# Kernel tuning notes

Measured on AMD Instinct MI355X. Metric: run time of the kernel, lower is better.

Reference implementation:

```python
import jax, jax.numpy as jnp
import numpy as np


def _spectral_norm(W, u):
    # W: [out, in] (1x1 conv weight flattened), u: [out]
    # one power-iteration step (torch does this under no_grad), then
    # sigma = u' @ W @ v with gradient flowing through W only.
    v = W.T @ u
    v = v / jnp.linalg.norm(v)
    u2 = W @ v
    u2 = u2 / jnp.linalg.norm(u2)
    v = jax.lax.stop_gradient(v)
    u2 = jax.lax.stop_gradient(u2)
    sigma = u2 @ (W @ v)
    return W / sigma


def setup_inputs() -> dict:
    key = jax.random.key(0)
    ks = jax.random.split(key, 8)
    B, C, H, W = 32, 512, 32, 32
    Cq = C // 8  # 64
    x = jax.random.normal(ks[0], (B, C, H, W), dtype=jnp.float32)
    s = 1.0 / np.sqrt(C)
    return {
        "x": x,
        "Wq": jax.random.normal(ks[1], (Cq, C), dtype=jnp.float32) * s,
        "bq": jnp.zeros((Cq,), dtype=jnp.float32),
        "uq": jax.random.normal(ks[2], (Cq,), dtype=jnp.float32),
        "Wk": jax.random.normal(ks[3], (Cq, C), dtype=jnp.float32) * s,
        "bk": jnp.zeros((Cq,), dtype=jnp.float32),
        "uk": jax.random.normal(ks[4], (Cq,), dtype=jnp.float32),
        "Wv": jax.random.normal(ks[5], (C, C), dtype=jnp.float32) * s,
        "bv": jnp.zeros((C,), dtype=jnp.float32),
        "uv": jax.random.normal(ks[6], (C,), dtype=jnp.float32),
        "gamma": jnp.float32(0.5),
    }


def reference(x, Wq, bq, uq, Wk, bk, uk, Wv, bv, uv, gamma):
    B, C, H, W = x.shape
    N = H * W
    f = x.reshape(B, C, N)                                   # [B,C,N]
    # 1x1 conv == channel matmul with spectral-normalized weights
    q = jnp.einsum('oc,bcn->bno', _spectral_norm(Wq, uq), f) + bq          # [B,N,Cq]
    k = jnp.einsum('oc,bcn->bon', _spectral_norm(Wk, uk), f) + bk[:, None]  # [B,Cq,N]
    v = jnp.einsum('oc,bcn->bon', _spectral_norm(Wv, uv), f) + bv[:, None]  # [B,C,N]
    qk = jnp.einsum('bno,bom->bnm', q, k)                    # [B,N,N], no 1/sqrt(d)
    attn = jax.nn.softmax(qk, axis=1)                        # softmax over QUERY axis (dim 1)
    o = jnp.einsum('bcn,bnm->bcm', v, attn).reshape(B, C, H, W)
    return gamma * o + x
```

## Files before the change

### kernel.cpp

```cpp
#include <hip/hip_runtime.h>
#include <hip/hip_bf16.h>

typedef __hip_bfloat16 bf16;
typedef __bf16 bf16x8 __attribute__((ext_vector_type(8)));
typedef float  f32x4  __attribute__((ext_vector_type(4)));
typedef unsigned short u16x8 __attribute__((ext_vector_type(8)));

#define C_IN  512
#define N_SP  1024
#define BATCH 32

__device__ __forceinline__ float ldmix(const void* p, size_t i, int f32) {
    return f32 ? ((const float*)p)[i] : __bfloat162float(((const bf16*)p)[i]);
}
__device__ __forceinline__ void stmix(void* p, size_t i, float v, int f32) {
    if (f32) ((float*)p)[i] = v;
    else     ((bf16*)p)[i] = __float2bfloat16(v);
}
__device__ __forceinline__ unsigned short bfbits(float f) {
    bf16 t = __float2bfloat16(f);
    return *reinterpret_cast<unsigned short*>(&t);
}
__device__ __forceinline__ float bf2f(unsigned short h) {
    union { unsigned u; float f; } c; c.u = ((unsigned)h) << 16; return c.f;
}
__device__ __forceinline__ void ldvec8(const void* W, size_t base, int f32, float v[8]) {
    if (f32) {
        const float4* p = reinterpret_cast<const float4*>((const float*)W + base);
        float4 a = p[0], b = p[1];
        v[0] = a.x; v[1] = a.y; v[2] = a.z; v[3] = a.w;
        v[4] = b.x; v[5] = b.y; v[6] = b.z; v[7] = b.w;
    } else {
        u16x8 h = *reinterpret_cast<const u16x8*>((const bf16*)W + base);
#pragma unroll
        for (int j = 0; j < 8; ++j) v[j] = bf2f(h[j]);
    }
}

__device__ __forceinline__ void gload_lds16(const bf16* g, void* l) {
    __builtin_amdgcn_global_load_lds(
        (__attribute__((address_space(1))) void*)(g),
        (__attribute__((address_space(3))) void*)(l),
        16, 0, 0);
}

#define STAGE64(LDS, GROW, GPITCH, K0) do {                                    \
    int _c = (wave << 6) + lane; int _r = _c >> 2;                             \
    int _s = (_c & 3) ^ ((_r >> 1) & 3);                                       \
    gload_lds16((GROW) + (size_t)_r * (GPITCH) + (K0) + _s * 8,                \
                (char*)(LDS) + (wave << 10));                                  \
} while (0)

__device__ __forceinline__ bf16x8 swz_frag(const void* tile, int row, int quad) {
    return *(const bf16x8*)((const char*)tile + (row << 6) +
                            ((quad ^ ((row >> 1) & 3)) << 4));
}

#define STG256(LBASE, GROW, GPITCH, K0) do {                                   \
    _Pragma("unroll")                                                          \
    for (int _i = 0; _i < 4; ++_i) {                                           \
        int _c = ((wave * 4 + _i) << 6) + lane;                                \
        int _r = _c >> 3;                                                      \
        int _lc = (_c & 7) ^ (_r & 7);                                         \
        gload_lds16((GROW) + (size_t)_r * (GPITCH) + (K0) + _lc * 8,           \
                    (char*)(LBASE) + ((wave * 4 + _i) << 10));                 \
    }                                                                          \
} while (0)

__device__ __forceinline__ bf16x8 frag64(const void* tile, int row, int c8) {
    return *(const bf16x8*)((const char*)tile + (row << 7) +
                            ((c8 ^ (row & 7)) << 4));
}

__device__ __forceinline__ void tile_decode(int bid, int nblk, int& z, int& mc) {
    int GBk = nblk >> 5;
    if ((GBk & 7) == 0) {
        z  = (bid & 7) + 8 * ((bid >> 3) >> 5);
        mc = (bid >> 3) & 31;
    } else {
        z  = bid >> 5;
        mc = bid & 31;
    }
}
__device__ __forceinline__ void tile_decode8(int bid, int nblk, int& z, int& mc) {
    int GBk = nblk >> 3;
    if ((GBk & 7) == 0) {
        z  = (bid & 7) + 8 * (bid >> 6);
        mc = (bid >> 3) & 7;
    } else {
        z  = bid >> 3;
        mc = bid & 7;
    }
}

__global__ void k_detect(const unsigned short* __restrict__ xh, int* __restrict__ flag)
{
    __shared__ int red[256];
    int tid = threadIdx.x;
    unsigned short h = xh[2 * tid];
    int e = (h >> 7) & 0xFF;
    red[tid] = (e == 0 || (e >= 96 && e <= 159)) ? 1 : 0;
    __syncthreads();
    for (int s = 128; s > 0; s >>= 1) { if (tid < s) red[tid] += red[tid + s]; __syncthreads(); }
    if (tid == 0) *flag = (red[0] < 192) ? 1 : 0;
}

__global__ __launch_bounds__(256) void k_sn1(
    const void* __restrict__ Wq, const void* __restrict__ uq,
    const void* __restrict__ Wk, const void* __restrict__ uk,
    const void* __restrict__ Wv, const void* __restrict__ uv,
    const int* __restrict__ flag, float* __restrict__ tpart)
{
    __shared__ float sh_u[64];
    __shared__ float sh_acc[4][512];
    int f32 = *flag;
    int bx = blockIdx.x;
    const void *W, *u; int oc, slot;
    if (bx == 0)      { W = Wq; u = uq; oc = 0;      slot = 0; }
    else if (bx == 1) { W = Wk; u = uk; oc = 0;      slot = 1; }
    else              { W = Wv; u = uv; oc = bx - 2; slot = bx; }
    int tid = threadIdx.x, wave = tid >> 6, lane = tid & 63;
    if (tid < 64) sh_u[tid] = ldmix(u, oc * 64 + tid, f32);
    __syncthreads();

    float acc[8];
#pragma unroll
    for (int j = 0; j < 8; ++j) acc[j] = 0.f;
    int obase = oc * 64 + wave * 16;
#pragma unroll 4
    for (int i = 0; i < 16; ++i) {
        int o = obase + i;
        float w8[8]; ldvec8(W, (size_t)o * C_IN + lane * 8, f32, w8);
        float uo = sh_u[o - oc * 64];
#pragma unroll
        for (int j = 0; j < 8; ++j) acc[j] += w8[j] * uo;
    }
#pragma unroll
    for (int j = 0; j < 8; ++j) sh_acc[wave][lane * 8 + j] = acc[j];
    __syncthreads();
    for (int c = tid; c < 512; c += 256)
        tpart[(size_t)slot * 512 + c] =
            sh_acc[0][c] + sh_acc[1][c] + sh_acc[2][c] + sh_acc[3][c];
}

__global__ __launch_bounds__(512) void k_sn2(
    const void* __restrict__ Wq, const void* __restrict__ Wk,
    const void* __restrict__ Wv, const int* __restrict__ flag,
    const float* __restrict__ tpart, float* __restrict__ sig)
{
    __shared__ float sh_t[512];
    __shared__ float red[512];
    int f32 = *flag;
    int m = blockIdx.x;
    const void* W; int out, slot0, nch;
    if (m == 0)      { W = Wq; out = 64;  slot0 = 0; nch = 1; }
    else if (m == 1) { W = Wk; out = 64;  slot0 = 1; nch = 1; }
    else             { W = Wv; out = 512; slot0 = 2; nch = 8; }
    int tid = threadIdx.x, wave = tid >> 6, lane = tid & 63;

    float t = 0.f;
    for (int c2 = 0; c2 < nch; ++c2) t += tpart[(size_t)(slot0 + c2) * 512 + tid];
    sh_t[tid] = t;
    red[tid] = t * t;
    __syncthreads();
    for (int s = 256; s > 0; s >>= 1) { if (tid < s) red[tid] += red[tid + s]; __syncthreads(); }
    float t2 = red[0];
    __syncthreads();

    float tl[8];
#pragma unroll
    for (int j = 0; j < 8; ++j) tl[j] = sh_t[lane * 8 + j];

    float s2 = 0.f;
#pragma unroll 2
    for (int o = wave; o < out; o += 8) {
        float w8[8]; ldvec8(W, (size_t)o * C_IN + lane * 8, f32, w8);
        float d = 0.f;
#pragma unroll
        for (int j = 0; j < 8; ++j) d += w8[j] * tl[j];
#pragma unroll
        for (int off = 32; off > 0; off >>= 1) d += __shfl_xor(d, off);
        if (lane == 0) s2 += d * d;
    }
    __syncthreads();
    red[tid] = (lane == 0) ? s2 : 0.f;
    __syncthreads();
    for (int s = 256; s > 0; s >>= 1) { if (tid < s) red[tid] += red[tid + s]; __syncthreads(); }
    if (tid == 0) sig[m] = sqrtf(t2 / red[0]);
}

__global__ __launch_bounds__(256) void k_wscale(
    const void* __restrict__ Wq, const void* __restrict__ bq,
    const void* __restrict__ Wk, const void* __restrict__ bk,
    const void* __restrict__ Wv, const void* __restrict__ bv,
    const float* __restrict__ sig, const int* __restrict__ flag,
    bf16* __restrict__ Wb, bf16* __restrict__ Wlo, float* __restrict__ biasf)
{
    int f32 = *flag;
    int r = blockIdx.x;
    const void *W, *b; int row; float s;
    if (r < 64)       { W = Wq; b = bq; row = r;       s = sig[0]; }
    else if (r < 128) { W = Wk; b = bk; row = r - 64;  s = sig[1]; }
    else              { W = Wv; b = bv; row = r - 128; s = sig[2]; }
    for (int c = threadIdx.x; c < C_IN; c += 256) {
        float w = ldmix(W, (size_t)row * C_IN + c, f32) * s;
        bf16 hi = __float2bfloat16(w);
        Wb[(size_t)r * C_IN + c] = hi;
        if (r < 128)
            Wlo[(size_t)r * C_IN + c] = __float2bfloat16(w - __bfloat162float(hi));
    }
    if (threadIdx.x == 0) biasf[r] = ldmix(b, row, f32);
}

__global__ __launch_bounds__(256) void k_xt(
    const void* __restrict__ x, const int* __restrict__ flag,
    char* __restrict__ SX, int batch0)
{
    __shared__ float tile[64][65];
    int f32 = *flag;
    int z = blockIdx.z;
    int n0 = blockIdx.x * 64, c0 = blockIdx.y * 64;
    size_t xoff = (size_t)(batch0 + z) * C_IN * N_SP;
    bf16* xTh = (bf16*)(SX + (size_t)z * 4194304);
    bf16* xTl = xTh + 524288;
    int tid = threadIdx.x;
#pragma unroll
    for (int i = 0; i < 4; ++i) {
        int idx = tid + i * 256;
        int c = idx >> 4, nq = idx & 15;
#pragma unroll
        for (int t = 0; t < 4; ++t)
            tile[c][nq * 4 + t] = ldmix(x, xoff + (size_t)(c0 + c) * N_SP + n0 + nq * 4 + t, f32);
    }
    __syncthreads();
#pragma unroll
    for (int i = 0; i < 16; ++i) {
        int idx = tid + i * 256;
        int n = idx >> 6, c = idx & 63;
        float v = tile[c][n];
        bf16 hi = __float2bfloat16(v);
        xTh[(size_t)(n0 + n) * C_IN + c0 + c] = hi;
        xTl[(size_t)(n0 + n) * C_IN + c0 + c] = __float2bfloat16(v - __bfloat162float(hi));
    }
}

__global__ __launch_bounds__(512, 1) void k_qkv_v(
    const bf16* __restrict__ Wb, const float* __restrict__ biasf,
    const char* __restrict__ SX, bf16* __restrict__ YV)
{
    extern __shared__ char lds[];
    int z, mc; tile_decode8(blockIdx.x, gridDim.x, z, mc);
    int r0 = 128 + (mc >> 2) * 256;
    int n0 = (mc & 3) * 256;
    const bf16* xTh = (const bf16*)(SX + (size_t)z * 4194304);
    bf16* Yv = YV + (size_t)z * 524288;
    int tid = threadIdx.x, wave = tid >> 6, lane = tid & 63, quad = lane >> 4, l16 = lane & 15;
    int wr = wave >> 2, wc4 = wave & 3;

    const bf16* Ar = Wb + (size_t)r0 * C_IN;
    const bf16* Br = xTh + (size_t)n0 * C_IN;

    f32x4 acc[8][4];
#pragma unroll
    for (int i = 0; i < 8; ++i)
#pragma unroll
        for (int j = 0; j < 4; ++j) acc[i][j] = (f32x4){0.f, 0.f, 0.f, 0.f};

    STG256(lds, Ar, C_IN, 0);
    STG256(lds + 32768, Br, C_IN, 0);
    asm volatile("s_waitcnt vmcnt(0)" ::: "memory");
    __builtin_amdgcn_s_barrier();
    __builtin_amdgcn_sched_barrier(0);

    for (int t = 0; t < 8; ++t) {
        const char* Ac = lds + (t & 1) * 65536;
        const char* Bc = Ac + 32768;
        if (t + 1 < 8) {
            char* An = lds + ((t + 1) & 1) * 65536;
            STG256(An, Ar, C_IN, (t + 1) * 64);
            STG256(An + 32768, Br, C_IN, (t + 1) * 64);
        }
#pragma unroll
        for (int kh = 0; kh < 2; ++kh) {
            bf16x8 af[8], bfr[4];
#pragma unroll
            for (int fm = 0; fm < 8; ++fm)
                af[fm] = frag64(Ac, wr * 128 + fm * 16 + l16, kh * 4 + quad);
#pragma unroll
            for (int fn = 0; fn < 4; ++fn)
                bfr[fn] = frag64(Bc, wc4 * 64 + fn * 16 + l16, kh * 4 + quad);
            __builtin_amdgcn_s_setprio(1);
#pragma unroll
            for (int fm = 0; fm < 8; ++fm)
#pragma unroll
                for (int fn = 0; fn < 4; ++fn)
                    acc[fm][fn] = __builtin_amdgcn_mfma_f32_16x16x32_bf16(af[fm], bfr[fn], acc[fm][fn], 0, 0, 0);
            __builtin_amdgcn_s_setprio(0);
        }
        asm volatile("s_waitcnt vmcnt(0)" ::: "memory");
        __builtin_amdgcn_s_barrier();
        __builtin_amdgcn_sched_barrier(0);
    }

#pragma unroll
    for (int fm = 0; fm < 8; ++fm)
#pragma unroll
        for (int fn = 0; fn < 4; ++fn)
#pragma unroll
            for (int r = 0; r < 4; ++r) {
                int c = r0 + wr * 128 + fm * 16 + quad * 4 + r;
                int n = n0 + wc4 * 64 + fn * 16 + l16;
                Yv[(size_t)(c - 128) * N_SP + n] = __float2bfloat16(acc[fm][fn][r] + biasf[c]);
            }
}

__global__ __launch_bounds__(256) void k_qkv_qk(
    const bf16* __restrict__ Wb, const bf16* __restrict__ Wlo,
    const float* __restrict__ biasf, const char* __restrict__ SX,
    bf16* __restrict__ QT, bf16* __restrict__ KT)
{
    __shared__ __bf16 Ah_[3][64][32], Al_[3][64][32], Bh_[3][64][32], Bl_[3][64][32];
    int z, mc; tile_decode(blockIdx.x, gridDim.x, z, mc);
    int n0 = (mc >> 1) * 64;
    int m0 = (mc & 1) * 64;
    const bf16* xTh = (const bf16*)(SX + (size_t)z * 4194304);
    const bf16* xTl = xTh + 524288;
    bf16* qt = QT + (size_t)z * 65536;
    bf16* kt = KT + (size_t)z * 65536;
    int tid = threadIdx.x, wave = tid >> 6, lane = tid & 63, quad = lane >> 4, l16 = lane & 15;
    int wmh = (wave >> 1) * 32, wnh = (wave & 1) * 32;

    const bf16* Ahr = Wb  + (size_t)m0 * C_IN;
    const bf16* Alr = Wlo + (size_t)m0 * C_IN;
    const bf16* Bhr = xTh + (size_t)n0 * C_IN;
    const bf16* Blr = xTl + (size_t)n0 * C_IN;

    f32x4 acc[2][2];
#pragma unroll
    for (int i = 0; i < 2; ++i)
#pragma unroll
        for (int j = 0; j < 2; ++j) acc[i][j] = (f32x4){0.f, 0.f, 0.f, 0.f};

    STAGE64(Ah_[0], Ahr, C_IN, 0);  STAGE64(Al_[0], Alr, C_IN, 0);
    STAGE64(Bh_[0], Bhr, C_IN, 0);  STAGE64(Bl_[0], Blr, C_IN, 0);
    STAGE64(Ah_[1], Ahr, C_IN, 32); STAGE64(Al_[1], Alr, C_IN, 32);
    STAGE64(Bh_[1], Bhr, C_IN, 32); STAGE64(Bl_[1], Blr, C_IN, 32);
    char *ah0 = (char*)Ah_[0], *ah1 = (char*)Ah_[1], *ah2 = (char*)Ah_[2];
    char *al0 = (char*)Al_[0], *al1 = (char*)Al_[1], *al2 = (char*)Al_[2];
    char *bh0 = (char*)Bh_[0], *bh1 = (char*)Bh_[1], *bh2 = (char*)Bh_[2];
    char *bl0 = (char*)Bl_[0], *bl1 = (char*)Bl_[1], *bl2 = (char*)Bl_[2];

#define QK_MFMA(PAH, PAL, PBH, PBL) {                                          \
    bf16x8 fah[2], fal[2], fbh[2], fbl[2];                                     \
    _Pragma("unroll")                                                          \
    for (int i = 0; i < 2; ++i) {                                              \
        fah[i] = swz_frag(PAH, wmh + i * 16 + l16, quad);                      \
        fal[i] = swz_frag(PAL, wmh + i * 16 + l16, quad);                      \
    }                                                                          \
    _Pragma("unroll")                                                          \
    for (int j = 0; j < 2; ++j) {                                              \
        fbh[j] = swz_frag(PBH, wnh + j * 16 + l16, quad);                      \
        fbl[j] = swz_frag(PBL, wnh + j * 16 + l16, quad);                      \
    }                                                                          \
    __builtin_amdgcn_s_setprio(1);                                             \
    _Pragma("unroll")                                                          \
    for (int i = 0; i < 2; ++i)                                                \
        _Pragma("unroll")                                                      \
        for (int j = 0; j < 2; ++j) {                                          \
            acc[i][j] = __builtin_amdgcn_mfma_f32_16x16x32_bf16(fah[i], fbh[j], acc[i][j], 0, 0, 0); \
            acc[i][j] = __builtin_amdgcn_mfma_f32_16x16x32_bf16(fah[i], fbl[j], acc[i][j], 0, 0, 0); \
            acc[i][j] = __builtin_amdgcn_mfma_f32_16x16x32_bf16(fal[i], fbh[j], acc[i][j], 0, 0, 0); \
        }                                                                      \
    __builtin_amdgcn_s_setprio(0); }

    for (int t = 0; t < 15; ++t) {
        asm volatile("s_waitcnt vmcnt(4)" ::: "memory");
        __builtin_amdgcn_s_barrier();
        __builtin_amdgcn_sched_barrier(0);
        if (t + 2 < 16) {
            int k2 = (t + 2) * 32;
            STAGE64(ah2, Ahr, C_IN, k2); STAGE64(al2, Alr, C_IN, k2);
            STAGE64(bh2, Bhr, C_IN, k2); STAGE64(bl2, Blr, C_IN, k2);
        }
        QK_MFMA(ah0, al0, bh0, bl0);
        char* tp = ah0; ah0 = ah1; ah1 = ah2; ah2 = tp;
        tp = al0; al0 = al1; al1 = al2; al2 = tp;
        tp = bh0; bh0 = bh1; bh1 = bh2; bh2 = tp;
        tp = bl0; bl0 = bl1; bl1 = bl2; bl2 = tp;
    }
    asm volatile("s_waitcnt vmcnt(0)" ::: "memory");
    __builtin_amdgcn_s_barrier();
    __builtin_amdgcn_sched_barrier(0);
    QK_MFMA(ah0, al0, bh0, bl0);
#undef QK_MFMA

#pragma unroll
    for (int i = 0; i < 2; ++i)
#pragma unroll
        for (int j = 0; j < 2; ++j) {
            int cbase = m0 + wmh + i * 16 + quad * 4;
            int n = n0 + wnh + j * 16 + l16;
            ushort4 st;
            st.x = bfbits(acc[i][j][0] + biasf[cbase + 0]);
            st.y = bfbits(acc[i][j][1] + biasf[cbase + 1]);
            st.z = bfbits(acc[i][j][2] + biasf[cbase + 2]);
            st.w = bfbits(acc[i][j][3] + biasf[cbase + 3]);
            bf16* dst = (m0 == 0) ? &qt[(size_t)n * 64 + cbase]
                                  : &kt[(size_t)n * 64 + (cbase - 64)];
            *reinterpret_cast<ushort4*>(dst) = st;
        }
}

__global__ __launch_bounds__(256) void k_qk(
    const bf16* __restrict__ QT, const bf16* __restrict__ KT,
    char* __restrict__ SX)
{
    __shared__ __bf16 Als[128][40];
    __shared__ __bf16 Bls[128][40];
    int z = blockIdx.z, m0 = blockIdx.y * 128, n0 = blockIdx.x * 128;
    const bf16* qt = QT + (size_t)z * 65536;
    const bf16* kt = KT + (size_t)z * 65536;
    float* Sf = (float*)(SX + (size_t)z * 4194304);
    int tid = threadIdx.x, wave = tid >> 6, lane = tid & 63, quad = lane >> 4, l16 = lane & 15;
    int wc = (wave >> 1) * 64, wm = (wave & 1) * 64;

    f32x4 acc[4][4];
#pragma unroll
    for (int i = 0; i < 4; ++i)
#pragma unroll
        for (int j = 0; j < 4; ++j) acc[i][j] = (f32x4){0.f, 0.f, 0.f, 0.f};

#pragma unroll
    for (int k0 = 0; k0 < 64; k0 += 32) {
#pragma unroll
        for (int s = 0; s < 2; ++s) {
            int idx = tid + s * 256; int row = idx >> 2, ch = idx & 3;
            *reinterpret_cast<uint4*>(&Als[row][ch * 8]) =
                *reinterpret_cast<const uint4*>(&kt[(size_t)(m0 + row) * 64 + k0 + ch * 8]);
            *reinterpret_cast<uint4*>(&Bls[row][ch * 8]) =
                *reinterpret_cast<const uint4*>(&qt[(size_t)(n0 + row) * 64 + k0 + ch * 8]);
        }
        __syncthreads();
        bf16x8 a[4], b[4];
#pragma unroll
        for (int i = 0; i < 4; ++i)
            a[i] = *reinterpret_cast<const bf16x8*>(&Als[wc + i * 16 + l16][quad * 8]);
#pragma unroll
        for (int j = 0; j < 4; ++j)
            b[j] = *reinterpret_cast<const bf16x8*>(&Bls[wm + j * 16 + l16][quad * 8]);
#pragma unroll
        for (int i = 0; i < 4; ++i)
#pragma unroll
            for (int j = 0; j < 4; ++j)
                acc[i][j] = __builtin_amdgcn_mfma_f32_16x16x32_bf16(a[i], b[j], acc[i][j], 0, 0, 0);
        __syncthreads();
    }
#pragma unroll
    for (int i = 0; i < 4; ++i)
#pragma unroll
        for (int j = 0; j < 4; ++j)
#pragma unroll
            for (int r = 0; r < 4; ++r) {
                int m = m0 + wc + i * 16 + quad * 4 + r;
                int n = n0 + wm + j * 16 + l16;
                Sf[(size_t)m * N_SP + n] = acc[i][j][r];
            }
}

__global__ __launch_bounds__(256) void k_softmax(char* __restrict__ SX)
{
    __shared__ float red[256];
    int z = blockIdx.x >> 10, m = blockIdx.x & 1023;
    float* p = (float*)(SX + (size_t)z * 4194304) + (size_t)m * N_SP;
    bf16* pb = (bf16*)p;
    int tid = threadIdx.x;
    float v0 = p[tid], v1 = p[tid + 256], v2 = p[tid + 512], v3 = p[tid + 768];
    red[tid] = fmaxf(fmaxf(v0, v1), fmaxf(v2, v3));
    __syncthreads();
    for (int s = 128; s > 0; s >>= 1) { if (tid < s) red[tid] = fmaxf(red[tid], red[tid + s]); __syncthreads(); }
    float mx = red[0];
    __syncthreads();
    float d0 = fmaxf(fminf(v0 - mx, 0.f), -80.f);
    float d1 = fmaxf(fminf(v1 - mx, 0.f), -80.f);
    float d2 = fmaxf(fminf(v2 - mx, 0.f), -80.f);
    float d3 = fmaxf(fminf(v3 - mx, 0.f), -80.f);
    float e0 = __expf(d0), e1 = __expf(d1), e2 = __expf(d2), e3 = __expf(d3);
    red[tid] = e0 + e1 + e2 + e3;
    __syncthreads();
    for (int s = 128; s > 0; s >>= 1) { if (tid < s) red[tid] += red[tid + s]; __syncthreads(); }
    float inv = 1.f / red[0];
    pb[tid]       = __float2bfloat16(e0 * inv);
    pb[tid + 256] = __float2bfloat16(e1 * inv);
    pb[tid + 512] = __float2bfloat16(e2 * inv);
    pb[tid + 768] = __float2bfloat16(e3 * inv);
}

__global__ __launch_bounds__(512, 1) void k_out(
    const bf16* __restrict__ YV, const char* __restrict__ SX,
    const void* __restrict__ x, const void* __restrict__ gamma,
    const int* __restrict__ flag, void* __restrict__ out, int batch0)
{
    extern __shared__ char lds[];
    int f32 = *flag;
    int z, mc; tile_decode8(blockIdx.x, gridDim.x, z, mc);
    int c0 = (mc >> 2) * 256;
    int m0 = (mc & 3) * 256;
    const bf16* Yv = YV + (size_t)z * 524288;
    const bf16* Pb = (const bf16*)(SX + (size_t)z * 4194304);
    int tid = threadIdx.x, wave = tid >> 6, lane = tid & 63, quad = lane >> 4, l16 = lane & 15;
    int wr = wave >> 2, wc4 = wave & 3;

    const bf16* Ar = Yv + (size_t)c0 * N_SP;
    const bf16* Br = Pb + (size_t)m0 * 2048;

    f32x4 acc[8][4];
#pragma unroll
    for (int i = 0; i < 8; ++i)
#pragma unroll
        for (int j = 0; j < 4; ++j) acc[i][j] = (f32x4){0.f, 0.f, 0.f, 0.f};

    STG256(lds, Ar, N_SP, 0);
    STG256(lds + 32768, Br, 2048, 0);
    asm volatile("s_waitcnt vmcnt(0)" ::: "memory");
    __builtin_amdgcn_s_barrier();
    __builtin_amdgcn_sched_barrier(0);

    for (int t = 0; t < 16; ++t) {
        const char* Ac = lds + (t & 1) * 65536;
        const char* Bc = Ac + 32768;
        if (t + 1 < 16) {
            char* An = lds + ((t + 1) & 1) * 65536;
            STG256(An, Ar, N_SP, (t + 1) * 64);
            STG256(An + 32768, Br, 2048, (t + 1) * 64);
        }
#pragma unroll
        for (int kh = 0; kh < 2; ++kh) {
            bf16x8 af[8], bfr[4];
#pragma unroll
            for (int fm = 0; fm < 8; ++fm)
                af[fm] = frag64(Ac, wr * 128 + fm * 16 + l16, kh * 4 + quad);
#pragma unroll
            for (int fn = 0; fn < 4; ++fn)
                bfr[fn] = frag64(Bc, wc4 * 64 + fn * 16 + l16, kh * 4 + quad);
            __builtin_amdgcn_s_setprio(1);
#pragma unroll
            for (int fm = 0; fm < 8; ++fm)
#pragma unroll
                for (int fn = 0; fn < 4; ++fn)
                    acc[fm][fn] = __builtin_amdgcn_mfma_f32_16x16x32_bf16(af[fm], bfr[fn], acc[fm][fn], 0, 0, 0);
            __builtin_amdgcn_s_setprio(0);
        }
        asm volatile("s_waitcnt vmcnt(0)" ::: "memory");
        __builtin_amdgcn_s_barrier();
        __builtin_amdgcn_sched_barrier(0);
    }

    float g = ldmix(gamma, 0, f32);
    const size_t base = (size_t)(batch0 + z) * C_IN * N_SP;
#pragma unroll
    for (int fm = 0; fm < 8; ++fm)
#pragma unroll
        for (int fn = 0; fn < 4; ++fn)
#pragma unroll
            for (int r = 0; r < 4; ++r) {
                int c = c0 + wr * 128 + fm * 16 + quad * 4 + r;
                int m = m0 + wc4 * 64 + fn * 16 + l16;
                size_t o = base + (size_t)c * N_SP + m;
                float v = fmaf(g, acc[fm][fn][r], ldmix(x, o, f32));
                if (!(v == v)) v = 5555.0f + 1000.0f * f32;
                stmix(out, o, v, f32);
            }
}

__global__ void k_wsfail(float* __restrict__ out, int n)
{
    int i = blockIdx.x * 256 + threadIdx.x;
    if (i < n) out[i] = 7777.0f;
}

extern "C" void kernel_launch(void* const* d_in, const int* in_sizes, int n_in,
                              void* d_out, int out_size, void* d_ws, size_t ws_size,
                              hipStream_t stream)
{
    const void* x  = d_in[0];
    const void* Wq = d_in[1];
    const void* bq = d_in[2];
    const void* Wk = d_in[4];
    const void* bk = d_in[5];
    const void* Wv = d_in[7];
    const void* bv = d_in[8];
    const void* uq = d_in[3];
    const void* uk = d_in[6];
    const void* uv = d_in[9];
    const void* gm = d_in[10];

    static int lds_opt_done = 0;
    if (!lds_opt_done) {
        (void)hipFuncSetAttribute(reinterpret_cast<const void*>(k_qkv_v),
                                  hipFuncAttributeMaxDynamicSharedMemorySize, 131072);
        (void)hipFuncSetAttribute(reinterpret_cast<const void*>(k_out),
                                  hipFuncAttributeMaxDynamicSharedMemorySize, 131072);
        lds_opt_done = 1;
    }

    const size_t HDR = 790528;
    const size_t per = 4194304 + 131072 + 131072 + 1048576;
    int GB = 0;
    for (int g = 32; g >= 1; g >>= 1)
        if (HDR + (size_t)g * per <= ws_size) { GB = g; break; }
    if (GB == 0) {
        k_wsfail<<<(out_size + 255) / 256, 256, 0, stream>>>((float*)d_out, out_size);
        return;
    }
    char* ws = (char*)d_ws;
    int*   flag  = (int*)ws;
    float* sig   = (float*)(ws + 16);
    float* biasf = (float*)(ws + 256);
    bf16*  Wb    = (bf16*)(ws + 4096);
    bf16*  Wlo   = (bf16*)(ws + 659456);
    char*  SX    = ws + HDR;
    bf16*  QT    = (bf16*)(SX + (size_t)GB * 4194304);
    bf16*  KT    = QT + (size_t)GB * 65536;
    bf16*  YV    = KT + (size_t)GB * 65536;
    float* tpart = (float*)SX;

    k_detect<<<1, 256, 0, stream>>>((const unsigned short*)x, flag);
    k_sn1<<<10, 256, 0, stream>>>(Wq, uq, Wk, uk, Wv, uv, flag, tpart);
    k_sn2<<<3, 512, 0, stream>>>(Wq, Wk, Wv, flag, tpart, sig);
    k_wscale<<<640, 256, 0, stream>>>(Wq, bq, Wk, bk, Wv, bv, sig, flag, Wb, Wlo, biasf);
    for (int b0 = 0; b0 < BATCH; b0 += GB) {
        k_xt     <<<dim3(16, 8, GB), 256, 0, stream>>>(x, flag, SX, b0);
        k_qkv_v  <<<GB * 8, 512, 131072, stream>>>(Wb, biasf, SX, YV);
        k_qkv_qk <<<GB * 32, 256, 0, stream>>>(Wb, Wlo, biasf, SX, QT, KT);
        k_qk     <<<dim3(8, 8, GB), 256, 0, stream>>>(QT, KT, SX);
        k_softmax<<<GB * 1024, 256, 0, stream>>>(SX);
        k_out    <<<GB * 8, 512, 131072, stream>>>(YV, SX, x, gm, flag, d_out, b0);
    }
}
```

Baseline: 393.3 us.

## Split GEMM k-tiles into 32-wide units with vmcnt(4) prefetch pipelining

Two 256x256 GEMM kernels (V projection and the V·attention output) now stage K in 32-wide units, four units in flight across two double-buffer slots. Each half-step waits with vmcnt(4) instead of draining all loads, so the next unit's global->LDS copy overlaps compute. A-fragment loads are split into two halves of four to cut register pressure and interleave LDS reads with MFMAs. This adds a barrier per half-step and relies on vmcnt counting being exact for correctness.

```diff
diff --git a/kernel.cpp b/kernel.cpp
--- a/kernel.cpp
+++ b/kernel.cpp
@@ -56,21 +56,35 @@
                             ((quad ^ ((row >> 1) & 3)) << 4));
 }
 
-#define STG256(LBASE, GROW, GPITCH, K0) do {                                   \
+#define STGUNIT(SLOT, AROW, APITCH, BROW, BPITCH, KOFF) do {                   \
+    char* _ub = lds + (size_t)(SLOT) * 32768;                                  \
     _Pragma("unroll")                                                          \
-    for (int _i = 0; _i < 4; ++_i) {                                           \
-        int _c = ((wave * 4 + _i) << 6) + lane;                                \
-        int _r = _c >> 3;                                                      \
-        int _lc = (_c & 7) ^ (_r & 7);                                         \
-        gload_lds16((GROW) + (size_t)_r * (GPITCH) + (K0) + _lc * 8,           \
-                    (char*)(LBASE) + ((wave * 4 + _i) << 10));                 \
+    for (int _i = 0; _i < 2; ++_i) {                                           \
+        int _c = ((wave * 2 + _i) << 6) + lane;                                \
+        int _r = _c >> 2; int _s = (_c & 3) ^ ((_r >> 1) & 3);                 \
+        gload_lds16((AROW) + (size_t)_r * (APITCH) + (KOFF) + _s * 8,          \
+                    _ub + ((wave * 2 + _i) << 10));                            \
+    }                                                                          \
+    _Pragma("unroll")                                                          \
+    for (int _i = 0; _i < 2; ++_i) {                                           \
+        int _c = ((wave * 2 + _i) << 6) + lane;                                \
+        int _r = _c >> 2; int _s = (_c & 3) ^ ((_r >> 1) & 3);                 \
+        gload_lds16((BROW) + (size_t)_r * (BPITCH) + (KOFF) + _s * 8,          \
+                    _ub + 16384 + ((wave * 2 + _i) << 10));                    \
     }                                                                          \
 } while (0)
 
-__device__ __forceinline__ bf16x8 frag64(const void* tile, int row, int c8) {
-    return *(const bf16x8*)((const char*)tile + (row << 7) +
-                            ((c8 ^ (row & 7)) << 4));
-}
+__device__ __forceinline__ bf16x8 frag32(const char* part, int row, int quad) {
+    return *(const bf16x8*)(part + (row << 6) +
+                            ((quad ^ ((row >> 1) & 3)) << 4));
+}
+
+#define WAIT4_BARRIER() do {                                                   \
+    asm volatile("s_waitcnt vmcnt(4)" ::: "memory");                           \
+    __builtin_amdgcn_sched_barrier(0);                                         \
+    __builtin_amdgcn_s_barrier();                                              \
+    __builtin_amdgcn_sched_barrier(0);                                         \
+} while (0)
 
 __device__ __forceinline__ void tile_decode(int bid, int nblk, int& z, int& mc) {
     int GBk = nblk >> 5;
@@ -266,40 +280,44 @@
 #pragma unroll
         for (int j = 0; j < 4; ++j) acc[i][j] = (f32x4){0.f, 0.f, 0.f, 0.f};
 
-    STG256(lds, Ar, C_IN, 0);
-    STG256(lds + 32768, Br, C_IN, 0);
-    asm volatile("s_waitcnt vmcnt(0)" ::: "memory");
-    __builtin_amdgcn_s_barrier();
-    __builtin_amdgcn_sched_barrier(0);
-
-    for (int t = 0; t < 8; ++t) {
-        const char* Ac = lds + (t & 1) * 65536;
-        const char* Bc = Ac + 32768;
-        if (t + 1 < 8) {
-            char* An = lds + ((t + 1) & 1) * 65536;
-            STG256(An, Ar, C_IN, (t + 1) * 64);
-            STG256(An + 32768, Br, C_IN, (t + 1) * 64);
-        }
+    STGUNIT(0, Ar, C_IN, Br, C_IN, 0);
+    STGUNIT(1, Ar, C_IN, Br, C_IN, 32);
+
+    const int NT = 8;
+    for (int t = 0; t < NT; ++t) {
+        int d = t & 1;
 #pragma unroll
         for (int kh = 0; kh < 2; ++kh) {
-            bf16x8 af[8], bfr[4];
-#pragma unroll
-            for (int fm = 0; fm < 8; ++fm)
-                af[fm] = frag64(Ac, wr * 128 + fm * 16 + l16, kh * 4 + quad);
+            const char* unit = lds + (size_t)(d * 2 + kh) * 32768;
+            WAIT4_BARRIER();
+            if (t + 1 < NT)
+                STGUNIT((d ^ 1) * 2 + kh, Ar, C_IN, Br, C_IN, (t + 1) * 64 + kh * 32);
+            bf16x8 bfr[4];
 #pragma unroll
             for (int fn = 0; fn < 4; ++fn)
-                bfr[fn] = frag64(Bc, wc4 * 64 + fn * 16 + l16, kh * 4 + quad);
+                bfr[fn] = frag32(unit + 16384, wc4 * 64 + fn * 16 + l16, quad);
+            bf16x8 af[4];
+#pragma unroll
+            for (int fm = 0; fm < 4; ++fm)
+                af[fm] = frag32(unit, wr * 128 + fm * 16 + l16, quad);
             __builtin_amdgcn_s_setprio(1);
 #pragma unroll
-            for (int fm = 0; fm < 8; ++fm)
+            for (int fm = 0; fm < 4; ++fm)
 #pragma unroll
                 for (int fn = 0; fn < 4; ++fn)
                     acc[fm][fn] = __builtin_amdgcn_mfma_f32_16x16x32_bf16(af[fm], bfr[fn], acc[fm][fn], 0, 0, 0);
             __builtin_amdgcn_s_setprio(0);
+#pragma unroll
+            for (int fm = 0; fm < 4; ++fm)
+                af[fm] = frag32(unit, wr * 128 + (fm + 4) * 16 + l16, quad);
+            __builtin_amdgcn_s_setprio(1);
+#pragma unroll
+            for (int fm = 0; fm < 4; ++fm)
+#pragma unroll
+                for (int fn = 0; fn < 4; ++fn)
+                    acc[fm + 4][fn] = __builtin_amdgcn_mfma_f32_16x16x32_bf16(af[fm], bfr[fn], acc[fm + 4][fn], 0, 0, 0);
+            __builtin_amdgcn_s_setprio(0);
         }
-        asm volatile("s_waitcnt vmcnt(0)" ::: "memory");
-        __builtin_amdgcn_s_barrier();
-        __builtin_amdgcn_sched_barrier(0);
     }
 
 #pragma unroll
@@ -519,40 +537,44 @@
 #pragma unroll
         for (int j = 0; j < 4; ++j) acc[i][j] = (f32x4){0.f, 0.f, 0.f, 0.f};
 
-    STG256(lds, Ar, N_SP, 0);
-    STG256(lds + 32768, Br, 2048, 0);
-    asm volatile("s_waitcnt vmcnt(0)" ::: "memory");
-    __builtin_amdgcn_s_barrier();
-    __builtin_amdgcn_sched_barrier(0);
-
-    for (int t = 0; t < 16; ++t) {
-        const char* Ac = lds + (t & 1) * 65536;
-        const char* Bc = Ac + 32768;
-        if (t + 1 < 16) {
-            char* An = lds + ((t + 1) & 1) * 65536;
-            STG256(An, Ar, N_SP, (t + 1) * 64);
-            STG256(An + 32768, Br, 2048, (t + 1) * 64);
-        }
+    STGUNIT(0, Ar, N_SP, Br, 2048, 0);
+    STGUNIT(1, Ar, N_SP, Br, 2048, 32);
+
+    const int NT = 16;
+    for (int t = 0; t < NT; ++t) {
+        int d = t & 1;
 #pragma unroll
         for (int kh = 0; kh < 2; ++kh) {
-            bf16x8 af[8], bfr[4];
-#pragma unroll
-            for (int fm = 0; fm < 8; ++fm)
-                af[fm] = frag64(Ac, wr * 128 + fm * 16 + l16, kh * 4 + quad);
+            const char* unit = lds + (size_t)(d * 2 + kh) * 32768;
+            WAIT4_BARRIER();
+            if (t + 1 < NT)
+                STGUNIT((d ^ 1) * 2 + kh, Ar, N_SP, Br, 2048, (t + 1) * 64 + kh * 32);
+            bf16x8 bfr[4];
 #pragma unroll
             for (int fn = 0; fn < 4; ++fn)
-                bfr[fn] = frag64(Bc, wc4 * 64 + fn * 16 + l16, kh * 4 + quad);
+                bfr[fn] = frag32(unit + 16384, wc4 * 64 + fn * 16 + l16, quad);
+            bf16x8 af[4];
+#pragma unroll
+            for (int fm = 0; fm < 4; ++fm)
+                af[fm] = frag32(unit, wr * 128 + fm * 16 + l16, quad);
             __builtin_amdgcn_s_setprio(1);
 #pragma unroll
-            for (int fm = 0; fm < 8; ++fm)
+            for (int fm = 0; fm < 4; ++fm)
 #pragma unroll
                 for (int fn = 0; fn < 4; ++fn)
                     acc[fm][fn] = __builtin_amdgcn_mfma_f32_16x16x32_bf16(af[fm], bfr[fn], acc[fm][fn], 0, 0, 0);
             __builtin_amdgcn_s_setprio(0);
+#pragma unroll
+            for (int fm = 0; fm < 4; ++fm)
+                af[fm] = frag32(unit, wr * 128 + (fm + 4) * 16 + l16, quad);
+            __builtin_amdgcn_s_setprio(1);
+#pragma unroll
+            for (int fm = 0; fm < 4; ++fm)
+#pragma unroll
+                for (int fn = 0; fn < 4; ++fn)
+                    acc[fm + 4][fn] = __builtin_amdgcn_mfma_f32_16x16x32_bf16(af[fm], bfr[fn], acc[fm + 4][fn], 0, 0, 0);
+            __builtin_amdgcn_s_setprio(0);
         }
-        asm volatile("s_waitcnt vmcnt(0)" ::: "memory");
-        __builtin_amdgcn_s_barrier();
-        __builtin_amdgcn_sched_barrier(0);
     }
 
     float g = ldmix(gamma, 0, f32);
```

Measured after the change: 396.7 us. About the same (+0.9%).
